# Performance work log

Hardware: AMD Instinct MI355X
Metric: run time of the kernel (lower is better)

## Reference

```python
import jax, jax.numpy as jnp
import numpy as np

VOCAB, EMB, NDIM, B, T = 50000, 300, 512, 128, 128


def gru_cell(x, h, Wih, Whh, bih, bhh):
    # torch nn.GRU gate order: [r, z, n]
    gi = x @ Wih.T + bih
    gh = h @ Whh.T + bhh
    i_r, i_z, i_n = jnp.split(gi, 3, axis=-1)
    h_r, h_z, h_n = jnp.split(gh, 3, axis=-1)
    r = jax.nn.sigmoid(i_r + h_r)
    z = jax.nn.sigmoid(i_z + h_z)
    n = jnp.tanh(i_n + r * h_n)
    return (1.0 - z) * n + z * h


def masked_gru(X, mask, h0, Wih, Whh, bih, bhh):
    # X: T x B x d, mask: T x B, h0: B x n. Replicates _gru_forward:
    # step-0 output is stored UNmasked (o_tm1 is None), later steps blend.
    h_raw = gru_cell(X[0], h0, Wih, Whh, bih, bhh)
    m0 = mask[0][:, None]
    h = h_raw * m0 + h0 * (1.0 - m0)
    o = h_raw

    def step(carry, inp):
        h, o = carry
        x_t, m_t = inp
        m = m_t[:, None]
        hr = gru_cell(x_t, h, Wih, Whh, bih, bhh)
        h_new = hr * m + h * (1.0 - m)
        o_new = hr * m + o * (1.0 - m)
        return (h_new, o_new), o_new

    (h_f, _), o_rest = jax.lax.scan(step, (h, o), (X[1:], mask[1:]))
    return jnp.concatenate([o[None], o_rest], axis=0), h_f


def rte_forward(premise, hypothesis, E, p_Wih, p_Whh, p_bih, p_bhh,
                h_Wih, h_Whh, h_bih, h_bhh, m_Wih, m_Whh, m_bih, m_bhh,
                W_y, W_h, W_r, W_alpha, out_W, out_b):
    bsz = premise.shape[0]
    n_dim = W_y.shape[0]
    mask_p = (premise != 0).astype(E.dtype).T            # T x B
    mask_h = (hypothesis != 0).astype(E.dtype).T
    enc_p = E[premise].transpose(1, 0, 2)                # T x B x EMB (eval: no dropout)
    enc_h = E[hypothesis].transpose(1, 0, 2)
    h0 = jnp.zeros((bsz, n_dim), dtype=E.dtype)
    o_p, h_n = masked_gru(enc_p, mask_p, h0, p_Wih, p_Whh, p_bih, p_bhh)
    o_h, _ = masked_gru(enc_h, mask_h, h_n, h_Wih, h_Whh, h_bih, h_bhh)

    Y = o_p.transpose(1, 0, 2)                           # B x Tp x n
    Yw = Y @ W_y                                         # hoisted: constant across steps
    maskY = mask_p.T                                     # B x Tp

    def step(r, inp):
        h_t, m_t = inp
        s = h_t @ W_h + r @ W_r                          # B x n
        M = jnp.tanh(Yw + s[:, None, :])                 # B x Tp x n
        alpha = (M @ W_alpha)[..., 0]                    # B x Tp
        alpha = alpha - 1000.0 * (1.0 - maskY)
        alpha = jax.nn.softmax(alpha, axis=-1)
        a = jnp.einsum('bt,btn->bn', alpha, Y)
        m_in = jnp.concatenate([a, h_t], axis=-1)        # B x 2n
        rr = gru_cell(m_in, r, m_Wih, m_Whh, m_bih, m_bhh)
        m = m_t[:, None]
        r_new = rr * m + r * (1.0 - m)
        return r_new, alpha

    r0 = jnp.zeros((bsz, n_dim), dtype=E.dtype)
    r_f, _alpha_vec = jax.lax.scan(step, r0, (o_h, mask_h))
    logits = r_f @ out_W.T + out_b                       # B x 3
    return jax.nn.log_softmax(logits, axis=-1)


def setup_inputs():
    key = jax.random.key(0)
    ks = jax.random.split(key, 22)
    s = 0.05
    def rn(k, sh):
        return jax.random.normal(k, sh, dtype=jnp.float32) * s
    G = 3 * NDIM
    return {
        "premise": jax.random.randint(ks[0], (B, T), 0, VOCAB),
        "hypothesis": jax.random.randint(ks[1], (B, T), 0, VOCAB),
        "E": rn(ks[2], (VOCAB, EMB)),
        "p_Wih": rn(ks[3], (G, EMB)), "p_Whh": rn(ks[4], (G, NDIM)),
        "p_bih": rn(ks[5], (G,)), "p_bhh": rn(ks[6], (G,)),
        "h_Wih": rn(ks[7], (G, EMB)), "h_Whh": rn(ks[8], (G, NDIM)),
        "h_bih": rn(ks[9], (G,)), "h_bhh": rn(ks[10], (G,)),
        "m_Wih": rn(ks[11], (G, 2 * NDIM)), "m_Whh": rn(ks[12], (G, NDIM)),
        "m_bih": rn(ks[13], (G,)), "m_bhh": rn(ks[14], (G,)),
        "W_y": rn(ks[15], (NDIM, NDIM)), "W_h": rn(ks[16], (NDIM, NDIM)),
        "W_r": rn(ks[17], (NDIM, NDIM)), "W_alpha": rn(ks[18], (NDIM, 1)),
        "out_W": rn(ks[19], (3, NDIM)), "out_b": rn(ks[20], (3,)),
    }


def reference(premise, hypothesis, E, p_Wih, p_Whh, p_bih, p_bhh,
              h_Wih, h_Whh, h_bih, h_bhh, m_Wih, m_Whh, m_bih, m_bhh,
              W_y, W_h, W_r, W_alpha, out_W, out_b):
    return rte_forward(premise, hypothesis, E, p_Wih, p_Whh, p_bih, p_bhh,
                       h_Wih, h_Whh, h_bih, h_bhh, m_Wih, m_Whh, m_bih, m_bhh,
                       W_y, W_h, W_r, W_alpha, out_W, out_b)
```

## Files before the change

### kernel.cpp

```cpp
#include <hip/hip_runtime.h>
#include <math.h>

#define B_SZ 128
#define T_SZ 128
#define EMBD 300
#define ND 512
#define G3 1536
#define FPAD 32

typedef short s16x8 __attribute__((ext_vector_type(8)));
typedef float f32x4 __attribute__((ext_vector_type(4)));
typedef unsigned long long u64;

__device__ __forceinline__ unsigned short f2b(float x) {
    unsigned u = __float_as_uint(x);
    unsigned r = (u + 0x7fff + ((u >> 16) & 1)) >> 16;
    return (unsigned short)r;
}
__device__ __forceinline__ float b2f(unsigned short v) {
    return __uint_as_float(((unsigned)v) << 16);
}
__device__ __forceinline__ float fsigmoid(float x) { return 1.0f / (1.0f + __expf(-x)); }
__device__ __forceinline__ float ftanh(float x) { return 1.0f - 2.0f / (__expf(2.0f * x) + 1.0f); }

__device__ __forceinline__ f32x4 mfma16(s16x8 a, s16x8 b, f32x4 c) {
    return __builtin_amdgcn_mfma_f32_16x16x32_bf16(a, b, c, 0, 0, 0);
}

__device__ __forceinline__ u64 cld64(const void* p) {
    return __hip_atomic_load((const u64*)p, __ATOMIC_RELAXED, __HIP_MEMORY_SCOPE_AGENT);
}
__device__ __forceinline__ void cst64(void* p, u64 v) {
    __hip_atomic_store((u64*)p, v, __ATOMIC_RELAXED, __HIP_MEMORY_SCOPE_AGENT);
}
__device__ __forceinline__ unsigned cld32(const void* p) {
    return __hip_atomic_load((const unsigned*)p, __ATOMIC_RELAXED, __HIP_MEMORY_SCOPE_AGENT);
}
__device__ __forceinline__ void cst32(void* p, unsigned v) {
    __hip_atomic_store((unsigned*)p, v, __ATOMIC_RELAXED, __HIP_MEMORY_SCOPE_AGENT);
}
__device__ __forceinline__ s16x8 cld_frag(const unsigned short* p) {
    union { u64 q[2]; s16x8 v; } u;
    u.q[0] = cld64(p);
    u.q[1] = cld64(p + 4);
    return u.v;
}

__device__ __forceinline__ void waitflags(const unsigned* f, int n, unsigned ep)
{
    if (threadIdx.x < 64) {
#pragma unroll 1
        for (int i = threadIdx.x; i < n; i += 64)
            while (cld32(&f[(long)i * FPAD]) < ep)
                __builtin_amdgcn_s_sleep(2);
    }
    __syncthreads();
}

__device__ __forceinline__ void fbar(unsigned* flags, int nb, unsigned ep)
{
    __syncthreads();
    if (threadIdx.x == 0)
        cst32(&flags[(long)blockIdx.x * FPAD], ep);
    waitflags(flags, nb, ep);
}

template<typename AT, bool OB>
__global__ __launch_bounds__(256)
void mfma_gemm(const AT* __restrict__ A, const int* __restrict__ idxA,
               const unsigned short* __restrict__ Wb, const float* __restrict__ bias,
               void* __restrict__ Cv,
               int M, int N, int K, int ldA, int Kpad, int ldC)
{
    __shared__ unsigned short As[64][40];
    __shared__ unsigned short Bs[64][40];
    const int tid = threadIdx.x;
    const int wv = tid >> 6, lane = tid & 63;
    const int wm = wv >> 1, wn = wv & 1;
    const int m0 = blockIdx.y * 64, n0 = blockIdx.x * 64;

    f32x4 acc[2][2] = {{{0.f,0.f,0.f,0.f},{0.f,0.f,0.f,0.f}},
                       {{0.f,0.f,0.f,0.f},{0.f,0.f,0.f,0.f}}};
    const int r_st = tid >> 2, k_st = (tid & 3) * 8;

    long arow = -1;
    {
        int gm = m0 + r_st;
        if (gm < M) arow = idxA ? (long)idxA[gm] : (long)gm;
    }

    const int kIters = (K + 31) / 32;
    for (int it = 0; it < kIters; ++it) {
        const int kg = it * 32 + k_st;
        {
            s16x8 pk = {0,0,0,0,0,0,0,0};
            if (arow >= 0) {
                if constexpr (sizeof(AT) == 2) {
                    if (kg + 8 <= K) {
                        pk = *(const s16x8*)((const unsigned short*)A + arow * (long)ldA + kg);
                    } else {
#pragma unroll
                        for (int j = 0; j < 8; ++j)
                            if (kg + j < K) pk[j] = (short)((const unsigned short*)A)[arow * (long)ldA + kg + j];
                    }
                } else {
                    if (kg + 8 <= K) {
                        const float* p = (const float*)A + arow * (long)ldA + kg;
                        f32x4 u0 = *(const f32x4*)p;
                        f32x4 u1 = *(const f32x4*)(p + 4);
#pragma unroll
                        for (int j = 0; j < 4; ++j) { pk[j] = (short)f2b(u0[j]); pk[4+j] = (short)f2b(u1[j]); }
                    } else {
#pragma unroll
                        for (int j = 0; j < 8; ++j) {
                            int kk = kg + j;
                            if (kk < K) pk[j] = (short)f2b(((const float*)A)[arow * (long)ldA + kk]);
                        }
                    }
                }
            }
            *(s16x8*)&As[r_st][k_st] = pk;
        }
        {
            int gn = n0 + r_st;
            s16x8 pk = {0,0,0,0,0,0,0,0};
            if (gn < N) pk = *(const s16x8*)&Wb[(long)gn * Kpad + kg];
            *(s16x8*)&Bs[r_st][k_st] = pk;
        }
        __syncthreads();
        {
            const int koff = (lane >> 4) * 8;
            s16x8 af[2], bfr[2];
#pragma unroll
            for (int f = 0; f < 2; ++f) {
                af[f]  = *(s16x8*)&As[wm * 32 + f * 16 + (lane & 15)][koff];
                bfr[f] = *(s16x8*)&Bs[wn * 32 + f * 16 + (lane & 15)][koff];
            }
#pragma unroll
            for (int fi = 0; fi < 2; ++fi)
#pragma unroll
                for (int fj = 0; fj < 2; ++fj)
                    acc[fi][fj] = mfma16(af[fi], bfr[fj], acc[fi][fj]);
        }
        __syncthreads();
    }
#pragma unroll
    for (int fi = 0; fi < 2; ++fi)
#pragma unroll
        for (int fj = 0; fj < 2; ++fj)
#pragma unroll
            for (int r = 0; r < 4; ++r) {
                int m = m0 + wm * 32 + fi * 16 + (lane >> 4) * 4 + r;
                int n = n0 + wn * 32 + fj * 16 + (lane & 15);
                if (m < M && n < N) {
                    float v = acc[fi][fj][r];
                    if (bias) v += bias[n];
                    if constexpr (OB) ((unsigned short*)Cv)[(long)m * ldC + n] = f2b(v);
                    else               ((float*)Cv)[(long)m * ldC + n] = v;
                }
            }
}

#define GRU_NB 64
__global__ __launch_bounds__(256, 1)
void gru_chain(const unsigned short* __restrict__ Whh_b, const float* __restrict__ GI,
               const float* __restrict__ bhh, const int* __restrict__ toks,
               float* __restrict__ h32a, float* __restrict__ h32b,
               unsigned short* __restrict__ h16a, unsigned short* __restrict__ h16b,
               unsigned short* __restrict__ o_bt,
               unsigned* __restrict__ flags)
{
    __shared__ unsigned short wlds[3][16][512];
    __shared__ unsigned short ht[64][20];
    const int tid = threadIdx.x;
    const int wv = tid >> 6, lane = tid & 63;
    const int dt = blockIdx.x & 31, bh = blockIdx.x >> 5;
    const int b0 = bh * 64;

    for (int s = 0; s < 12; ++s) {
        int slot = tid + s * 256;
        int g = slot >> 10, rem = slot & 1023, ks = rem >> 6, ln = rem & 63;
        int row = g * ND + dt * 16 + (ln & 15);
        int k = ks * 32 + (ln >> 4) * 8;
        *(s16x8*)&wlds[g][ks][ln * 8] = *(const s16x8*)&Whh_b[(long)row * ND + k];
    }
    __syncthreads();

    const int d = dt * 16 + (lane & 15);
    const int brow = b0 + wv * 16 + (lane >> 4) * 4;
    const int arow = b0 + wv * 16 + (lane & 15);
    const int akoff = (lane >> 4) * 8;

    float o_run[4] = {0.f, 0.f, 0.f, 0.f};
    unsigned ep = 0;

    for (int t = 0; t < T_SZ; ++t) {
        const unsigned short* hin16 = (t & 1) ? h16b : h16a;
        const float*          hin32 = (t & 1) ? h32b : h32a;
        float*          hout32 = (t & 1) ? h32a : h32b;
        unsigned short* hout16 = (t & 1) ? h16a : h16b;

        const float* git = GI + (long)t * (B_SZ * G3);
        float gi_r[4], gi_z[4], gi_n[4], hp[4]; int mk[4];
#pragma unroll
        for (int rr = 0; rr < 4; ++rr) {
            int b = brow + rr;
            gi_r[rr] = git[(long)b * G3 + d];
            gi_z[rr] = git[(long)b * G3 + ND + d];
            gi_n[rr] = git[(long)b * G3 + 2 * ND + d];
            hp[rr]   = hin32[(long)b * ND + d];
            mk[rr]   = toks[b * T_SZ + t];
        }

        f32x4 acc0 = {0,0,0,0}, acc1 = {0,0,0,0}, acc2 = {0,0,0,0};
#pragma unroll
        for (int ks = 0; ks < 16; ++ks) {
            s16x8 a  = cld_frag(&hin16[(long)arow * ND + ks * 32 + akoff]);
            s16x8 br = *(s16x8*)&wlds[0][ks][lane * 8];
            s16x8 bz = *(s16x8*)&wlds[1][ks][lane * 8];
            s16x8 bn = *(s16x8*)&wlds[2][ks][lane * 8];
            acc0 = mfma16(a, br, acc0);
            acc1 = mfma16(a, bz, acc1);
            acc2 = mfma16(a, bn, acc2);
        }

#pragma unroll
        for (int rr = 0; rr < 4; ++rr) {
            int b = brow + rr;
            float rg = fsigmoid(gi_r[rr] + acc0[rr] + bhh[d]);
            float zg = fsigmoid(gi_z[rr] + acc1[rr] + bhh[ND + d]);
            float ng = ftanh(gi_n[rr] + rg * (acc2[rr] + bhh[2 * ND + d]));
            float hr = (1.0f - zg) * ng + zg * hp[rr];
            bool m = mk[rr] != 0;
            float hn = m ? hr : hp[rr];
            hout32[(long)b * ND + d] = hn;
            ht[b - b0][lane & 15] = f2b(hn);
            o_run[rr] = (t == 0) ? hr : (m ? hr : o_run[rr]);
            o_bt[((long)b * T_SZ + t) * ND + d] = f2b(o_run[rr]);
        }
        __syncthreads();
        {
            int bl = tid & 63, dq = tid >> 6;
            u64 v = *(u64*)&ht[bl][dq * 4];
            cst64(&hout16[(long)(b0 + bl) * ND + dt * 16 + dq * 4], v);
        }
        fbar(flags, GRU_NB, ++ep);
    }
}

#define UP_NB 32
#define YPITCH 520
__global__ __launch_bounds__(256, 1)
void match_chain(const unsigned short* __restrict__ WrT_b,
                 const unsigned short* __restrict__ mWihL_b,
                 const unsigned short* __restrict__ mWhh_b,
                 const unsigned short* __restrict__ OHWh_bt,
                 const unsigned short* __restrict__ OHGI_bt,
                 const float* __restrict__ m_bhh, const float* __restrict__ Walpha,
                 const unsigned short* __restrict__ Yw_bb,
                 const unsigned short* __restrict__ Y_bb,
                 const int* __restrict__ prem, const int* __restrict__ hyp,
                 float* __restrict__ r32,
                 unsigned short* __restrict__ r16a, unsigned short* __restrict__ r16b,
                 unsigned short* __restrict__ a16, unsigned short* __restrict__ s16,
                 unsigned* __restrict__ lflags, unsigned* __restrict__ uflags,
                 unsigned* __restrict__ sflags)
{
    __shared__ __align__(16) unsigned char smem[157696];
    const int tid = threadIdx.x;
    const int wv = tid >> 6, lane = tid & 63;

    if (blockIdx.x < 128) {
        const int b = blockIdx.x;
        unsigned short (*ywl)[YPITCH] = (unsigned short(*)[YPITCH])smem;
        float* wal  = (float*)(smem + 133120);
        float* sarr = (float*)(smem + 135168);
        float* part = (float*)(smem + 137216);
        float* lg   = (float*)(smem + 138240);
        float* red  = (float*)(smem + 138752);
        float* sr2  = (float*)(smem + 138784);

        for (int s = 0; s < 32; ++s) {
            int c = s * 256 + tid;
            int row = c >> 6, cg = c & 63;
            *(s16x8*)&ywl[row][cg * 8] =
                *(const s16x8*)&Yw_bb[((long)b * T_SZ + row) * ND + cg * 8];
        }
        if (tid < 128) {
            f32x4 w = *(const f32x4*)&Walpha[tid * 4];
            *(f32x4*)&wal[tid * 4] = w;
        }
        __syncthreads();

        const int tp = tid >> 1, gh = tid & 1;
        const unsigned short* yrow = &ywl[tp][gh * 256];
        const float* sp  = &sarr[gh * 256];
        const float* wap = &wal[gh * 256];

        for (int t = 0; t < T_SZ; ++t) {
            waitflags(sflags, UP_NB, (unsigned)(t + 1));
            if (tid < 64) {
                s16x8 q = cld_frag(&s16[(long)b * ND + tid * 8]);
#pragma unroll
                for (int j = 0; j < 8; ++j) sarr[tid * 8 + j] = b2f((unsigned short)q[j]);
            }
            __syncthreads();
            {
                float acc = 0.f;
#pragma unroll 4
                for (int i8 = 0; i8 < 32; ++i8) {
                    s16x8 yw = *(const s16x8*)&yrow[i8 * 8];
                    f32x4 s0 = *(const f32x4*)&sp[i8 * 8];
                    f32x4 s1 = *(const f32x4*)&sp[i8 * 8 + 4];
                    f32x4 w0 = *(const f32x4*)&wap[i8 * 8];
                    f32x4 w1 = *(const f32x4*)&wap[i8 * 8 + 4];
#pragma unroll
                    for (int j = 0; j < 4; ++j)
                        acc += ftanh(b2f((unsigned short)yw[j]) + s0[j]) * w0[j];
#pragma unroll
                    for (int j = 0; j < 4; ++j)
                        acc += ftanh(b2f((unsigned short)yw[4 + j]) + s1[j]) * w1[j];
                }
                part[tid] = acc;
            }
            __syncthreads();
            if (tid < 128) {
                float v = part[tid * 2] + part[tid * 2 + 1];
                float mm = (prem[b * T_SZ + tid] != 0) ? 0.f : 1000.f;
                lg[tid] = v - mm;
            }
            __syncthreads();
            if (tid < 64) {
                float v = fmaxf(lg[tid], lg[tid + 64]);
#pragma unroll
                for (int off = 32; off; off >>= 1) v = fmaxf(v, __shfl_xor(v, off));
                if (tid == 0) red[0] = v;
            }
            __syncthreads();
            float mx = red[0];
            if (tid < T_SZ) lg[tid] = __expf(lg[tid] - mx);
            __syncthreads();
            if (tid < 64) {
                float v = lg[tid] + lg[tid + 64];
#pragma unroll
                for (int off = 32; off; off >>= 1) v += __shfl_xor(v, off);
                if (tid == 0) red[1] = v;
            }
            __syncthreads();
            float inv = 1.0f / red[1];
            int g = tid >> 7, lt = tid & 127, n4 = lt * 4;
            f32x4 acw = {0.f, 0.f, 0.f, 0.f};
#pragma unroll 8
            for (int i = 0; i < 64; ++i) {
                int tpp = g * 64 + i;
                float al = lg[tpp] * inv;
                u64 q = *(const u64*)&Y_bb[((long)b * T_SZ + tpp) * ND + n4];
                acw[0] += al * b2f((unsigned short)q);
                acw[1] += al * b2f((unsigned short)(q >> 16));
                acw[2] += al * b2f((unsigned short)(q >> 32));
                acw[3] += al * b2f((unsigned short)(q >> 48));
            }
            if (g == 1) *(f32x4*)&sr2[n4] = acw;
            __syncthreads();
            if (g == 0) {
                f32x4 o = *(f32x4*)&sr2[n4];
                u64 pk = (u64)f2b(acw[0] + o[0]) | ((u64)f2b(acw[1] + o[1]) << 16)
                       | ((u64)f2b(acw[2] + o[2]) << 32) | ((u64)f2b(acw[3] + o[3]) << 48);
                cst64(&a16[(long)b * ND + n4], pk);
            }
            __syncthreads();
            if (tid == 0) cst32(&lflags[(long)b * FPAD], (unsigned)(t + 1));
        }
    } else {
        const int ug = blockIdx.x - 128;
        unsigned short (*wA)[16][512] = (unsigned short(*)[16][512])smem;
        unsigned short (*wR)[16][512] = (unsigned short(*)[16][512])(smem + 49152);
        float (*bounce)[84] = (float(*)[84])(smem + 49152 + 65536);

        for (int s = 0; s < 12; ++s) {
            int slot = tid + s * 256;
            int fam = slot >> 10, rem = slot & 1023, ks = rem >> 6, ln = rem & 63;
            int row = fam * ND + ug * 16 + (ln & 15);
            int k = ks * 32 + (ln >> 4) * 8;
            *(s16x8*)&wA[fam][ks][ln * 8] = *(const s16x8*)&mWihL_b[(long)row * ND + k];
        }
        for (int s = 0; s < 16; ++s) {
            int slot = tid + s * 256;
            int fam = slot >> 10, rem = slot & 1023, ks = rem >> 6, ln = rem & 63;
            int k = ks * 32 + (ln >> 4) * 8;
            const unsigned short* src = (fam < 3)
                ? &mWhh_b[(long)(fam * ND + ug * 16 + (ln & 15)) * ND + k]
                : &WrT_b[(long)(ug * 16 + (ln & 15)) * ND + k];
            *(s16x8*)&wR[fam][ks][ln * 8] = *(const s16x8*)src;
        }
        __syncthreads();

        const int akoff = (lane >> 4) * 8;
        const int cb = tid >> 1;
        const int half = tid & 1;
        const int d0 = ug * 16 + half * 8;

        for (int t = 0; t < T_SZ; ++t) {
            waitflags(uflags, UP_NB, (unsigned)t);
            const unsigned short* r16rd = (t & 1) ? r16b : r16a;
            unsigned short*       r16wr = (t & 1) ? r16a : r16b;

            f32x4 aSR[2] = {{0,0,0,0},{0,0,0,0}}, aSZ[2] = {{0,0,0,0},{0,0,0,0}};
            f32x4 aHN[2] = {{0,0,0,0},{0,0,0,0}}, aS[2]  = {{0,0,0,0},{0,0,0,0}};
            f32x4 aGN[2] = {{0,0,0,0},{0,0,0,0}};
#pragma unroll
            for (int f = 0; f < 2; ++f) {
                int row = wv * 32 + f * 16 + (lane & 15);
#pragma unroll
                for (int ks = 0; ks < 16; ++ks) {
                    s16x8 a = cld_frag(&r16rd[(long)row * ND + ks * 32 + akoff]);
                    aSR[f] = mfma16(a, *(s16x8*)&wR[0][ks][lane * 8], aSR[f]);
                    aSZ[f] = mfma16(a, *(s16x8*)&wR[1][ks][lane * 8], aSZ[f]);
                    aHN[f] = mfma16(a, *(s16x8*)&wR[2][ks][lane * 8], aHN[f]);
                    aS[f]  = mfma16(a, *(s16x8*)&wR[3][ks][lane * 8], aS[f]);
                }
            }
#pragma unroll
            for (int f = 0; f < 2; ++f)
#pragma unroll
                for (int rr = 0; rr < 4; ++rr)
                    bounce[wv * 32 + f * 16 + (lane >> 4) * 4 + rr][64 + (lane & 15)] = aS[f][rr];
            __syncthreads();
            {
                u64 qa = *(const u64*)&OHWh_bt[((long)cb * T_SZ + t) * ND + d0];
                u64 qb = *(const u64*)&OHWh_bt[((long)cb * T_SZ + t) * ND + d0 + 4];
                u64 w0 = 0, w1 = 0;
#pragma unroll
                for (int j = 0; j < 4; ++j) {
                    float v0 = bounce[cb][64 + half * 8 + j]     + b2f((unsigned short)(qa >> (16 * j)));
                    float v1 = bounce[cb][64 + half * 8 + 4 + j] + b2f((unsigned short)(qb >> (16 * j)));
                    w0 |= (u64)f2b(v0) << (16 * j);
                    w1 |= (u64)f2b(v1) << (16 * j);
                }
                cst64(&s16[(long)cb * ND + d0], w0);
                cst64(&s16[(long)cb * ND + d0 + 4], w1);
            }
            __syncthreads();
            if (tid == 0) cst32(&sflags[(long)ug * FPAD], (unsigned)(t + 1));

            waitflags(lflags, 128, (unsigned)(t + 1));
#pragma unroll
            for (int f = 0; f < 2; ++f) {
                int row = wv * 32 + f * 16 + (lane & 15);
#pragma unroll
                for (int ks = 0; ks < 16; ++ks) {
                    s16x8 a = cld_frag(&a16[(long)row * ND + ks * 32 + akoff]);
                    aSR[f] = mfma16(a, *(s16x8*)&wA[0][ks][lane * 8], aSR[f]);
                    aSZ[f] = mfma16(a, *(s16x8*)&wA[1][ks][lane * 8], aSZ[f]);
                    aGN[f] = mfma16(a, *(s16x8*)&wA[2][ks][lane * 8], aGN[f]);
                }
            }
#pragma unroll
            for (int f = 0; f < 2; ++f)
#pragma unroll
                for (int rr = 0; rr < 4; ++rr) {
                    int bb = wv * 32 + f * 16 + (lane >> 4) * 4 + rr;
                    bounce[bb][0  + (lane & 15)] = aSR[f][rr];
                    bounce[bb][16 + (lane & 15)] = aSZ[f][rr];
                    bounce[bb][32 + (lane & 15)] = aGN[f][rr];
                    bounce[bb][48 + (lane & 15)] = aHN[f][rr];
                }
            __syncthreads();
            {
                const unsigned short* og = OHGI_bt + ((long)cb * T_SZ + t) * G3;
                u64 q0a = *(const u64*)&og[d0];            u64 q0b = *(const u64*)&og[d0 + 4];
                u64 q1a = *(const u64*)&og[ND + d0];       u64 q1b = *(const u64*)&og[ND + d0 + 4];
                u64 q2a = *(const u64*)&og[2 * ND + d0];   u64 q2b = *(const u64*)&og[2 * ND + d0 + 4];
                f32x4 rpA = *(const f32x4*)&r32[(long)cb * ND + d0];
                f32x4 rpB = *(const f32x4*)&r32[(long)cb * ND + d0 + 4];
                bool mkk = hyp[cb * T_SZ + t] != 0;
                u64 w0 = 0, w1 = 0;
#pragma unroll
                for (int j = 0; j < 8; ++j) {
                    int dl = half * 8 + j;
                    int dd = ug * 16 + dl;
                    u64 qg0 = (j < 4) ? q0a : q0b;
                    u64 qg1 = (j < 4) ? q1a : q1b;
                    u64 qg2 = (j < 4) ? q2a : q2b;
                    int sh = 16 * (j & 3);
                    float sr  = bounce[cb][0 + dl]  + b2f((unsigned short)(qg0 >> sh)) + m_bhh[dd];
                    float sz  = bounce[cb][16 + dl] + b2f((unsigned short)(qg1 >> sh)) + m_bhh[ND + dd];
                    float gin = bounce[cb][32 + dl] + b2f((unsigned short)(qg2 >> sh));
                    float ghn = bounce[cb][48 + dl] + m_bhh[2 * ND + dd];
                    float rg = fsigmoid(sr), zg = fsigmoid(sz);
                    float ng = ftanh(gin + rg * ghn);
                    float rp = (j < 4) ? rpA[j & 3] : rpB[j & 3];
                    float rn = (1.0f - zg) * ng + zg * rp;
                    float v = mkk ? rn : rp;
                    if (j < 4) rpA[j & 3] = v; else rpB[j & 3] = v;
                    if (j < 4) w0 |= (u64)f2b(v) << sh; else w1 |= (u64)f2b(v) << sh;
                }
                *(f32x4*)&r32[(long)cb * ND + d0] = rpA;
                *(f32x4*)&r32[(long)cb * ND + d0 + 4] = rpB;
                cst64(&r16wr[(long)cb * ND + d0], w0);
                cst64(&r16wr[(long)cb * ND + d0 + 4], w1);
            }
            __syncthreads();
            if (tid == 0) cst32(&uflags[(long)ug * FPAD], (unsigned)(t + 1));
        }
    }
}

__global__ void prep_idx(const int* __restrict__ prem, const int* __restrict__ hyp,
                         int* __restrict__ idx_p, int* __restrict__ idx_h)
{
    int i = blockIdx.x * blockDim.x + threadIdx.x;
    if (i < B_SZ * T_SZ) {
        int t = i / B_SZ, b = i % B_SZ;
        idx_p[i] = prem[b * T_SZ + t];
        idx_h[i] = hyp[b * T_SZ + t];
    }
}

__global__ void conv_w(const float* __restrict__ in, unsigned short* __restrict__ out,
                       int N, int K, int Kpad, int ldIn, int colOff)
{
    long i = (long)blockIdx.x * blockDim.x + threadIdx.x;
    if (i >= (long)N * Kpad) return;
    int n = (int)(i / Kpad), k = (int)(i % Kpad);
    float v = (k < K) ? in[(long)n * ldIn + k + colOff] : 0.0f;
    out[i] = f2b(v);
}

__global__ void conv_wT(const float* __restrict__ in, unsigned short* __restrict__ out,
                        int N, int K, int Kpad, int ldIn)
{
    long i = (long)blockIdx.x * blockDim.x + threadIdx.x;
    if (i >= (long)N * Kpad) return;
    int n = (int)(i / Kpad), k = (int)(i % Kpad);
    float v = (k < K) ? in[(long)k * ldIn + n] : 0.0f;
    out[i] = f2b(v);
}

__global__ void zero_kernel(float* __restrict__ p, int n)
{
    int i = blockIdx.x * blockDim.x + threadIdx.x;
    if (i < n) p[i] = 0.0f;
}

__global__ void final_logits(const float* __restrict__ r, const float* __restrict__ outW,
                             const float* __restrict__ outb, float* __restrict__ out)
{
    int b = blockIdx.x;
    int lane = threadIdx.x;
    float a0 = 0.0f, a1 = 0.0f, a2 = 0.0f;
    for (int k = lane; k < ND; k += 64) {
        float rv = r[(long)b * ND + k];
        a0 += rv * outW[0 * ND + k];
        a1 += rv * outW[1 * ND + k];
        a2 += rv * outW[2 * ND + k];
    }
#pragma unroll
    for (int off = 32; off; off >>= 1) {
        a0 += __shfl_down(a0, off);
        a1 += __shfl_down(a1, off);
        a2 += __shfl_down(a2, off);
    }
    if (lane == 0) {
        float l0 = a0 + outb[0], l1 = a1 + outb[1], l2 = a2 + outb[2];
        float mx = fmaxf(l0, fmaxf(l1, l2));
        float se = expf(l0 - mx) + expf(l1 - mx) + expf(l2 - mx);
        float ls = mx + logf(se);
        out[b * 3 + 0] = l0 - ls;
        out[b * 3 + 1] = l1 - ls;
        out[b * 3 + 2] = l2 - ls;
    }
}

extern "C" void kernel_launch(void* const* d_in, const int* in_sizes, int n_in,
                              void* d_out, int out_size, void* d_ws, size_t ws_size,
                              hipStream_t stream)
{
    const int*   prem    = (const int*)d_in[0];
    const int*   hyp     = (const int*)d_in[1];
    const float* E       = (const float*)d_in[2];
    const float* p_Wih   = (const float*)d_in[3];
    const float* p_Whh   = (const float*)d_in[4];
    const float* p_bih   = (const float*)d_in[5];
    const float* p_bhh   = (const float*)d_in[6];
    const float* h_Wih   = (const float*)d_in[7];
    const float* h_Whh   = (const float*)d_in[8];
    const float* h_bih   = (const float*)d_in[9];
    const float* h_bhh   = (const float*)d_in[10];
    const float* m_Wih   = (const float*)d_in[11];
    const float* m_Whh   = (const float*)d_in[12];
    const float* m_bih   = (const float*)d_in[13];
    const float* m_bhh   = (const float*)d_in[14];
    const float* W_y     = (const float*)d_in[15];
    const float* W_h     = (const float*)d_in[16];
    const float* W_r     = (const float*)d_in[17];
    const float* W_alpha = (const float*)d_in[18];
    const float* out_W   = (const float*)d_in[19];
    const float* out_b   = (const float*)d_in[20];
    float* out = (float*)d_out;

    const int MB = T_SZ * B_SZ;
    const int NFLAGS = 320 * FPAD;

    float* ws = (float*)d_ws;
    size_t off = 0;
    float* GI    = ws + off; off += (size_t)MB * G3;
    float* h32a  = ws + off; off += (size_t)B_SZ * ND;
    float* h32b  = ws + off; off += (size_t)B_SZ * ND;
    float* r32   = ws + off; off += (size_t)B_SZ * ND;
    unsigned* flags = (unsigned*)(ws + off); off += NFLAGS;
    int* idx_p = (int*)(ws + off); off += (size_t)B_SZ * T_SZ;
    int* idx_h = (int*)(ws + off); off += (size_t)B_SZ * T_SZ;
    unsigned short* ub = (unsigned short*)(ws + off);
    size_t uoff = 0;
    unsigned short* o_p_bt = ub + uoff; uoff += (size_t)MB * ND;
    unsigned short* o_h_bt = ub + uoff; uoff += (size_t)MB * ND;
    unsigned short* Yw_bb  = ub + uoff; uoff += (size_t)MB * ND;
    unsigned short* OHWh_bt= ub + uoff; uoff += (size_t)MB * ND;
    unsigned short* OHGI_bt= ub + uoff; uoff += (size_t)MB * G3;
    unsigned short* h16a   = ub + uoff; uoff += (size_t)B_SZ * ND;
    unsigned short* h16b   = ub + uoff; uoff += (size_t)B_SZ * ND;
    unsigned short* r16a   = ub + uoff; uoff += (size_t)B_SZ * ND;
    unsigned short* r16b   = ub + uoff; uoff += (size_t)B_SZ * ND;
    unsigned short* a16    = ub + uoff; uoff += (size_t)B_SZ * ND;
    unsigned short* s16    = ub + uoff; uoff += (size_t)B_SZ * ND;
    unsigned short* pWih_b = ub + uoff; uoff += (size_t)G3 * 320;
    unsigned short* hWih_b = ub + uoff; uoff += (size_t)G3 * 320;
    unsigned short* pWhh_b = ub + uoff; uoff += (size_t)G3 * ND;
    unsigned short* hWhh_b = ub + uoff; uoff += (size_t)G3 * ND;
    unsigned short* mWihL_b= ub + uoff; uoff += (size_t)G3 * ND;
    unsigned short* mWihR  = ub + uoff; uoff += (size_t)G3 * ND;
    unsigned short* mWhh_b = ub + uoff; uoff += (size_t)G3 * ND;
    unsigned short* WyT_b  = ub + uoff; uoff += (size_t)ND * ND;
    unsigned short* WhT_b  = ub + uoff; uoff += (size_t)ND * ND;
    unsigned short* WrT_b  = ub + uoff; uoff += (size_t)ND * ND;
    off += (uoff + 1) / 2;
    if (ws_size < off * sizeof(float)) return;

    auto cblk = [](long n) { return (int)((n + 255) / 256); };

    prep_idx<<<cblk(MB), 256, 0, stream>>>(prem, hyp, idx_p, idx_h);
    conv_w <<<cblk((long)G3 * 320), 256, 0, stream>>>(p_Wih, pWih_b, G3, EMBD, 320, EMBD, 0);
    conv_w <<<cblk((long)G3 * 320), 256, 0, stream>>>(h_Wih, hWih_b, G3, EMBD, 320, EMBD, 0);
    conv_w <<<cblk((long)G3 * ND), 256, 0, stream>>>(p_Whh, pWhh_b, G3, ND, ND, ND, 0);
    conv_w <<<cblk((long)G3 * ND), 256, 0, stream>>>(h_Whh, hWhh_b, G3, ND, ND, ND, 0);
    conv_w <<<cblk((long)G3 * ND), 256, 0, stream>>>(m_Wih, mWihL_b, G3, ND, ND, 2 * ND, 0);
    conv_w <<<cblk((long)G3 * ND), 256, 0, stream>>>(m_Wih, mWihR, G3, ND, ND, 2 * ND, ND);
    conv_w <<<cblk((long)G3 * ND), 256, 0, stream>>>(m_Whh, mWhh_b, G3, ND, ND, ND, 0);
    conv_wT<<<cblk((long)ND * ND), 256, 0, stream>>>(W_y, WyT_b, ND, ND, ND, ND);
    conv_wT<<<cblk((long)ND * ND), 256, 0, stream>>>(W_h, WhT_b, ND, ND, ND, ND);
    conv_wT<<<cblk((long)ND * ND), 256, 0, stream>>>(W_r, WrT_b, ND, ND, ND, ND);
    zero_kernel<<<cblk(B_SZ * ND), 256, 0, stream>>>(h32a, B_SZ * ND);
    zero_kernel<<<cblk(B_SZ * ND / 2), 256, 0, stream>>>((float*)h16a, B_SZ * ND / 2);
    zero_kernel<<<cblk(B_SZ * ND), 256, 0, stream>>>(r32, B_SZ * ND);
    zero_kernel<<<cblk(B_SZ * ND / 2), 256, 0, stream>>>((float*)r16a, B_SZ * ND / 2);
    zero_kernel<<<cblk(B_SZ * ND / 2), 256, 0, stream>>>((float*)r16b, B_SZ * ND / 2);
    zero_kernel<<<cblk(NFLAGS), 256, 0, stream>>>((float*)flags, NFLAGS);

    {
        dim3 g(G3 / 64, MB / 64);
        mfma_gemm<float, false><<<g, 256, 0, stream>>>(E, idx_p, pWih_b, p_bih, GI,
                                                       MB, G3, EMBD, EMBD, 320, G3);
    }
    gru_chain<<<GRU_NB, 256, 0, stream>>>(pWhh_b, GI, p_bhh, prem, h32a, h32b, h16a, h16b,
                                          o_p_bt, &flags[0]);

    {
        dim3 g(G3 / 64, MB / 64);
        mfma_gemm<float, false><<<g, 256, 0, stream>>>(E, idx_h, hWih_b, h_bih, GI,
                                                       MB, G3, EMBD, EMBD, 320, G3);
    }
    gru_chain<<<GRU_NB, 256, 0, stream>>>(hWhh_b, GI, h_bhh, hyp, h32a, h32b, h16a, h16b,
                                          o_h_bt, &flags[64 * FPAD]);

    {
        dim3 g(ND / 64, MB / 64);
        mfma_gemm<unsigned short, true><<<g, 256, 0, stream>>>(o_p_bt, nullptr, WyT_b, nullptr,
                                                               Yw_bb, MB, ND, ND, ND, ND, ND);
        mfma_gemm<unsigned short, true><<<g, 256, 0, stream>>>(o_h_bt, nullptr, WhT_b, nullptr,
                                                               OHWh_bt, MB, ND, ND, ND, ND, ND);
        dim3 g2(G3 / 64, MB / 64);
        mfma_gemm<unsigned short, true><<<g2, 256, 0, stream>>>(o_h_bt, nullptr, mWihR, m_bih,
                                                                OHGI_bt, MB, G3, ND, ND, ND, G3);
    }

    match_chain<<<160, 256, 0, stream>>>(WrT_b, mWihL_b, mWhh_b, OHWh_bt, OHGI_bt,
                                         m_bhh, W_alpha, Yw_bb, o_p_bt, prem, hyp,
                                         r32, r16a, r16b, a16, s16,
                                         &flags[128 * FPAD], &flags[256 * FPAD],
                                         &flags[288 * FPAD]);

    final_logits<<<B_SZ, 64, 0, stream>>>(r32, out_W, out_b, out);
}
```

Before: 7.348 ms.

## Replicate barrier flags, keep recurrent state in registers, prefetch step inputs

Each block now posts its barrier flag to eight replicated flag arrays and polls only its own replica. This spreads the spin-wait traffic on shared cache lines that sits on the critical path of every recurrent step. The GRU and match-update hidden states stay in registers and are written to global memory only at the final step. The match kernel drops the max-subtraction from its softmax, folds normalisation into the weighted sum, and hoists the mask. OHWh/OHGI are stored time-major so their loads can be issued before the wait; dropping the max-subtraction risks exp overflow for large logits.

```diff
diff --git a/kernel.cpp b/kernel.cpp
--- a/kernel.cpp
+++ b/kernel.cpp
@@ -7,6 +7,8 @@
 #define ND 512
 #define G3 1536
 #define FPAD 32
+#define NFID 320
+#define NREP 8
 
 typedef short s16x8 __attribute__((ext_vector_type(8)));
 typedef float f32x4 __attribute__((ext_vector_type(4)));
@@ -46,31 +48,42 @@
     return u.v;
 }
 
-__device__ __forceinline__ void waitflags(const unsigned* f, int n, unsigned ep)
-{
+__device__ __forceinline__ void postflag(unsigned* flags, int base, int id, unsigned ep)
+{
+    if (threadIdx.x < NREP)
+        cst32(&flags[((long)threadIdx.x * NFID + base + id) * FPAD], ep);
+}
+__device__ __forceinline__ void waitflags(const unsigned* flags, int base, int n,
+                                          unsigned ep, int rep)
+{
+    const unsigned* fr = flags + (long)rep * NFID * FPAD;
     if (threadIdx.x < 64) {
 #pragma unroll 1
         for (int i = threadIdx.x; i < n; i += 64)
-            while (cld32(&f[(long)i * FPAD]) < ep)
+            while (cld32(&fr[(long)(base + i) * FPAD]) < ep)
                 __builtin_amdgcn_s_sleep(2);
     }
     __syncthreads();
 }
-
-__device__ __forceinline__ void fbar(unsigned* flags, int nb, unsigned ep)
+__device__ __forceinline__ void fbar(unsigned* flags, int base, int nb, unsigned ep)
 {
     __syncthreads();
-    if (threadIdx.x == 0)
-        cst32(&flags[(long)blockIdx.x * FPAD], ep);
-    waitflags(flags, nb, ep);
-}
+    postflag(flags, base, blockIdx.x & 63, ep);
+    waitflags(flags, base, nb, ep, blockIdx.x & 7);
+}
+
+#define FB_GRUP 0
+#define FB_GRUH 64
+#define FB_LF   128
+#define FB_UF   256
+#define FB_SF   288
 
 template<typename AT, bool OB>
 __global__ __launch_bounds__(256)
 void mfma_gemm(const AT* __restrict__ A, const int* __restrict__ idxA,
                const unsigned short* __restrict__ Wb, const float* __restrict__ bias,
                void* __restrict__ Cv,
-               int M, int N, int K, int ldA, int Kpad, int ldC)
+               int M, int N, int K, int ldA, int Kpad, int ldC, int permC)
 {
     __shared__ unsigned short As[64][40];
     __shared__ unsigned short Bs[64][40];
@@ -155,8 +168,9 @@
                 if (m < M && n < N) {
                     float v = acc[fi][fj][r];
                     if (bias) v += bias[n];
-                    if constexpr (OB) ((unsigned short*)Cv)[(long)m * ldC + n] = f2b(v);
-                    else               ((float*)Cv)[(long)m * ldC + n] = v;
+                    long mo = permC ? ((long)(m & 127) * B_SZ + (m >> 7)) : (long)m;
+                    if constexpr (OB) ((unsigned short*)Cv)[mo * ldC + n] = f2b(v);
+                    else               ((float*)Cv)[mo * ldC + n] = v;
                 }
             }
 }
@@ -165,10 +179,10 @@
 __global__ __launch_bounds__(256, 1)
 void gru_chain(const unsigned short* __restrict__ Whh_b, const float* __restrict__ GI,
                const float* __restrict__ bhh, const int* __restrict__ toks,
-               float* __restrict__ h32a, float* __restrict__ h32b,
+               float* __restrict__ h32,
                unsigned short* __restrict__ h16a, unsigned short* __restrict__ h16b,
                unsigned short* __restrict__ o_bt,
-               unsigned* __restrict__ flags)
+               unsigned* __restrict__ flags, int fbase)
 {
     __shared__ unsigned short wlds[3][16][512];
     __shared__ unsigned short ht[64][20];
@@ -191,24 +205,25 @@
     const int arow = b0 + wv * 16 + (lane & 15);
     const int akoff = (lane >> 4) * 8;
 
+    float hreg[4];
+#pragma unroll
+    for (int rr = 0; rr < 4; ++rr) hreg[rr] = h32[(long)(brow + rr) * ND + d];
+
     float o_run[4] = {0.f, 0.f, 0.f, 0.f};
     unsigned ep = 0;
 
     for (int t = 0; t < T_SZ; ++t) {
         const unsigned short* hin16 = (t & 1) ? h16b : h16a;
-        const float*          hin32 = (t & 1) ? h32b : h32a;
-        float*          hout32 = (t & 1) ? h32a : h32b;
         unsigned short* hout16 = (t & 1) ? h16a : h16b;
 
         const float* git = GI + (long)t * (B_SZ * G3);
-        float gi_r[4], gi_z[4], gi_n[4], hp[4]; int mk[4];
+        float gi_r[4], gi_z[4], gi_n[4]; int mk[4];
 #pragma unroll
         for (int rr = 0; rr < 4; ++rr) {
             int b = brow + rr;
             gi_r[rr] = git[(long)b * G3 + d];
             gi_z[rr] = git[(long)b * G3 + ND + d];
             gi_n[rr] = git[(long)b * G3 + 2 * ND + d];
-            hp[rr]   = hin32[(long)b * ND + d];
             mk[rr]   = toks[b * T_SZ + t];
         }
 
@@ -230,11 +245,12 @@
             float rg = fsigmoid(gi_r[rr] + acc0[rr] + bhh[d]);
             float zg = fsigmoid(gi_z[rr] + acc1[rr] + bhh[ND + d]);
             float ng = ftanh(gi_n[rr] + rg * (acc2[rr] + bhh[2 * ND + d]));
-            float hr = (1.0f - zg) * ng + zg * hp[rr];
+            float hr = (1.0f - zg) * ng + zg * hreg[rr];
             bool m = mk[rr] != 0;
-            float hn = m ? hr : hp[rr];
-            hout32[(long)b * ND + d] = hn;
+            float hn = m ? hr : hreg[rr];
+            hreg[rr] = hn;
             ht[b - b0][lane & 15] = f2b(hn);
+            if (t == T_SZ - 1) h32[(long)b * ND + d] = hn;
             o_run[rr] = (t == 0) ? hr : (m ? hr : o_run[rr]);
             o_bt[((long)b * T_SZ + t) * ND + d] = f2b(o_run[rr]);
         }
@@ -244,18 +260,18 @@
             u64 v = *(u64*)&ht[bl][dq * 4];
             cst64(&hout16[(long)(b0 + bl) * ND + dt * 16 + dq * 4], v);
         }
-        fbar(flags, GRU_NB, ++ep);
+        fbar(flags, fbase, GRU_NB, ++ep);
     }
 }
 
 #define UP_NB 32
-#define YPITCH 520
+#define YPITCH 536
 __global__ __launch_bounds__(256, 1)
 void match_chain(const unsigned short* __restrict__ WrT_b,
                  const unsigned short* __restrict__ mWihL_b,
                  const unsigned short* __restrict__ mWhh_b,
-                 const unsigned short* __restrict__ OHWh_bt,
-                 const unsigned short* __restrict__ OHGI_bt,
+                 const unsigned short* __restrict__ OHWh_tb,
+                 const unsigned short* __restrict__ OHGI_tb,
                  const float* __restrict__ m_bhh, const float* __restrict__ Walpha,
                  const unsigned short* __restrict__ Yw_bb,
                  const unsigned short* __restrict__ Y_bb,
@@ -263,8 +279,7 @@
                  float* __restrict__ r32,
                  unsigned short* __restrict__ r16a, unsigned short* __restrict__ r16b,
                  unsigned short* __restrict__ a16, unsigned short* __restrict__ s16,
-                 unsigned* __restrict__ lflags, unsigned* __restrict__ uflags,
-                 unsigned* __restrict__ sflags)
+                 unsigned* __restrict__ flags)
 {
     __shared__ __align__(16) unsigned char smem[157696];
     const int tid = threadIdx.x;
@@ -272,13 +287,14 @@
 
     if (blockIdx.x < 128) {
         const int b = blockIdx.x;
+        const int rep = b & 7;
         unsigned short (*ywl)[YPITCH] = (unsigned short(*)[YPITCH])smem;
-        float* wal  = (float*)(smem + 133120);
-        float* sarr = (float*)(smem + 135168);
-        float* part = (float*)(smem + 137216);
-        float* lg   = (float*)(smem + 138240);
-        float* red  = (float*)(smem + 138752);
-        float* sr2  = (float*)(smem + 138784);
+        float* wal  = (float*)(smem + 137216);
+        float* sarr = (float*)(smem + 139264);
+        float* part = (float*)(smem + 141312);
+        float* lg   = (float*)(smem + 142336);
+        float* red  = (float*)(smem + 142848);
+        float* sr2  = (float*)(smem + 142880);
 
         for (int s = 0; s < 32; ++s) {
             int c = s * 256 + tid;
@@ -290,15 +306,18 @@
             f32x4 w = *(const f32x4*)&Walpha[tid * 4];
             *(f32x4*)&wal[tid * 4] = w;
         }
+        float mmreg = 0.f;
+        if (tid < 128) mmreg = (prem[b * T_SZ + tid] != 0) ? 0.f : 1000.f;
         __syncthreads();
 
         const int tp = tid >> 1, gh = tid & 1;
         const unsigned short* yrow = &ywl[tp][gh * 256];
         const float* sp  = &sarr[gh * 256];
         const float* wap = &wal[gh * 256];
+        const int g = tid >> 7, lt = tid & 127, n4 = lt * 4;
 
         for (int t = 0; t < T_SZ; ++t) {
-            waitflags(sflags, UP_NB, (unsigned)(t + 1));
+            waitflags(flags, FB_SF, UP_NB, (unsigned)(t + 1), rep);
             if (tid < 64) {
                 s16x8 q = cld_frag(&s16[(long)b * ND + tid * 8]);
 #pragma unroll
@@ -324,55 +343,39 @@
                 part[tid] = acc;
             }
             __syncthreads();
-            if (tid < 128) {
-                float v = part[tid * 2] + part[tid * 2 + 1];
-                float mm = (prem[b * T_SZ + tid] != 0) ? 0.f : 1000.f;
-                lg[tid] = v - mm;
-            }
-            __syncthreads();
-            if (tid < 64) {
-                float v = fmaxf(lg[tid], lg[tid + 64]);
-#pragma unroll
-                for (int off = 32; off; off >>= 1) v = fmaxf(v, __shfl_xor(v, off));
-                if (tid == 0) red[0] = v;
-            }
-            __syncthreads();
-            float mx = red[0];
-            if (tid < T_SZ) lg[tid] = __expf(lg[tid] - mx);
-            __syncthreads();
-            if (tid < 64) {
-                float v = lg[tid] + lg[tid + 64];
-#pragma unroll
-                for (int off = 32; off; off >>= 1) v += __shfl_xor(v, off);
-                if (tid == 0) red[1] = v;
-            }
-            __syncthreads();
-            float inv = 1.0f / red[1];
-            int g = tid >> 7, lt = tid & 127, n4 = lt * 4;
+            if (tid < 128) lg[tid] = __expf(part[tid * 2] + part[tid * 2 + 1] - mmreg);
+            __syncthreads();
+            float suml = 0.f;
             f32x4 acw = {0.f, 0.f, 0.f, 0.f};
 #pragma unroll 8
             for (int i = 0; i < 64; ++i) {
                 int tpp = g * 64 + i;
-                float al = lg[tpp] * inv;
+                float al = lg[tpp];
+                suml += al;
                 u64 q = *(const u64*)&Y_bb[((long)b * T_SZ + tpp) * ND + n4];
                 acw[0] += al * b2f((unsigned short)q);
                 acw[1] += al * b2f((unsigned short)(q >> 16));
                 acw[2] += al * b2f((unsigned short)(q >> 32));
                 acw[3] += al * b2f((unsigned short)(q >> 48));
             }
-            if (g == 1) *(f32x4*)&sr2[n4] = acw;
+            if (g == 1) {
+                *(f32x4*)&sr2[n4] = acw;
+                if (lt == 0) red[0] = suml;
+            }
             __syncthreads();
             if (g == 0) {
+                float inv = 1.0f / (suml + red[0]);
                 f32x4 o = *(f32x4*)&sr2[n4];
-                u64 pk = (u64)f2b(acw[0] + o[0]) | ((u64)f2b(acw[1] + o[1]) << 16)
-                       | ((u64)f2b(acw[2] + o[2]) << 32) | ((u64)f2b(acw[3] + o[3]) << 48);
+                u64 pk = (u64)f2b((acw[0] + o[0]) * inv) | ((u64)f2b((acw[1] + o[1]) * inv) << 16)
+                       | ((u64)f2b((acw[2] + o[2]) * inv) << 32) | ((u64)f2b((acw[3] + o[3]) * inv) << 48);
                 cst64(&a16[(long)b * ND + n4], pk);
             }
             __syncthreads();
-            if (tid == 0) cst32(&lflags[(long)b * FPAD], (unsigned)(t + 1));
+            postflag(flags, FB_LF, b, (unsigned)(t + 1));
         }
     } else {
         const int ug = blockIdx.x - 128;
+        const int rep = ug & 7;
         unsigned short (*wA)[16][512] = (unsigned short(*)[16][512])smem;
         unsigned short (*wR)[16][512] = (unsigned short(*)[16][512])(smem + 49152);
         float (*bounce)[84] = (float(*)[84])(smem + 49152 + 65536);
@@ -400,8 +403,19 @@
         const int half = tid & 1;
         const int d0 = ug * 16 + half * 8;
 
+        f32x4 rpA = {0,0,0,0}, rpB = {0,0,0,0};
+
         for (int t = 0; t < T_SZ; ++t) {
-            waitflags(uflags, UP_NB, (unsigned)t);
+            const unsigned short* ohw = &OHWh_tb[((long)t * B_SZ + cb) * ND + d0];
+            u64 qa = *(const u64*)ohw;
+            u64 qb = *(const u64*)(ohw + 4);
+            const unsigned short* og = &OHGI_tb[((long)t * B_SZ + cb) * G3];
+            u64 q0a = *(const u64*)&og[d0];            u64 q0b = *(const u64*)&og[d0 + 4];
+            u64 q1a = *(const u64*)&og[ND + d0];       u64 q1b = *(const u64*)&og[ND + d0 + 4];
+            u64 q2a = *(const u64*)&og[2 * ND + d0];   u64 q2b = *(const u64*)&og[2 * ND + d0 + 4];
+            int hv = hyp[cb * T_SZ + t];
+
+            waitflags(flags, FB_UF, UP_NB, (unsigned)t, rep);
             const unsigned short* r16rd = (t & 1) ? r16b : r16a;
             unsigned short*       r16wr = (t & 1) ? r16a : r16b;
 
@@ -427,8 +441,6 @@
                     bounce[wv * 32 + f * 16 + (lane >> 4) * 4 + rr][64 + (lane & 15)] = aS[f][rr];
             __syncthreads();
             {
-                u64 qa = *(const u64*)&OHWh_bt[((long)cb * T_SZ + t) * ND + d0];
-                u64 qb = *(const u64*)&OHWh_bt[((long)cb * T_SZ + t) * ND + d0 + 4];
                 u64 w0 = 0, w1 = 0;
 #pragma unroll
                 for (int j = 0; j < 4; ++j) {
@@ -441,9 +453,9 @@
                 cst64(&s16[(long)cb * ND + d0 + 4], w1);
             }
             __syncthreads();
-            if (tid == 0) cst32(&sflags[(long)ug * FPAD], (unsigned)(t + 1));
-
-            waitflags(lflags, 128, (unsigned)(t + 1));
+            postflag(flags, FB_SF, ug, (unsigned)(t + 1));
+
+            waitflags(flags, FB_LF, 128, (unsigned)(t + 1), rep);
 #pragma unroll
             for (int f = 0; f < 2; ++f) {
                 int row = wv * 32 + f * 16 + (lane & 15);
@@ -467,13 +479,7 @@
                 }
             __syncthreads();
             {
-                const unsigned short* og = OHGI_bt + ((long)cb * T_SZ + t) * G3;
-                u64 q0a = *(const u64*)&og[d0];            u64 q0b = *(const u64*)&og[d0 + 4];
-                u64 q1a = *(const u64*)&og[ND + d0];       u64 q1b = *(const u64*)&og[ND + d0 + 4];
-                u64 q2a = *(const u64*)&og[2 * ND + d0];   u64 q2b = *(const u64*)&og[2 * ND + d0 + 4];
-                f32x4 rpA = *(const f32x4*)&r32[(long)cb * ND + d0];
-                f32x4 rpB = *(const f32x4*)&r32[(long)cb * ND + d0 + 4];
-                bool mkk = hyp[cb * T_SZ + t] != 0;
+                bool mkk = hv != 0;
                 u64 w0 = 0, w1 = 0;
 #pragma unroll
                 for (int j = 0; j < 8; ++j) {
@@ -495,13 +501,15 @@
                     if (j < 4) rpA[j & 3] = v; else rpB[j & 3] = v;
                     if (j < 4) w0 |= (u64)f2b(v) << sh; else w1 |= (u64)f2b(v) << sh;
                 }
-                *(f32x4*)&r32[(long)cb * ND + d0] = rpA;
-                *(f32x4*)&r32[(long)cb * ND + d0 + 4] = rpB;
+                if (t == T_SZ - 1) {
+                    *(f32x4*)&r32[(long)cb * ND + d0] = rpA;
+                    *(f32x4*)&r32[(long)cb * ND + d0 + 4] = rpB;
+                }
                 cst64(&r16wr[(long)cb * ND + d0], w0);
                 cst64(&r16wr[(long)cb * ND + d0 + 4], w1);
             }
             __syncthreads();
-            if (tid == 0) cst32(&uflags[(long)ug * FPAD], (unsigned)(t + 1));
+            postflag(flags, FB_UF, ug, (unsigned)(t + 1));
         }
     }
 }
@@ -600,13 +608,12 @@
     float* out = (float*)d_out;
 
     const int MB = T_SZ * B_SZ;
-    const int NFLAGS = 320 * FPAD;
+    const int NFLAGS = NREP * NFID * FPAD;
 
     float* ws = (float*)d_ws;
     size_t off = 0;
     float* GI    = ws + off; off += (size_t)MB * G3;
-    float* h32a  = ws + off; off += (size_t)B_SZ * ND;
-    float* h32b  = ws + off; off += (size_t)B_SZ * ND;
+    float* h32   = ws + off; off += (size_t)B_SZ * ND;
     float* r32   = ws + off; off += (size_t)B_SZ * ND;
     unsigned* flags = (unsigned*)(ws + off); off += NFLAGS;
     int* idx_p = (int*)(ws + off); off += (size_t)B_SZ * T_SZ;
@@ -616,8 +623,8 @@
     unsigned short* o_p_bt = ub + uoff; uoff += (size_t)MB * ND;
     unsigned short* o_h_bt = ub + uoff; uoff += (size_t)MB * ND;
     unsigned short* Yw_bb  = ub + uoff; uoff += (size_t)MB * ND;
-    unsigned short* OHWh_bt= ub + uoff; uoff += (size_t)MB * ND;
-    unsigned short* OHGI_bt= ub + uoff; uoff += (size_t)MB * G3;
+    unsigned short* OHWh_tb= ub + uoff; uoff += (size_t)MB * ND;
+    unsigned short* OHGI_tb= ub + uoff; uoff += (size_t)MB * G3;
     unsigned short* h16a   = ub + uoff; uoff += (size_t)B_SZ * ND;
     unsigned short* h16b   = ub + uoff; uoff += (size_t)B_SZ * ND;
     unsigned short* r16a   = ub + uoff; uoff += (size_t)B_SZ * ND;
@@ -650,7 +657,7 @@
     conv_wT<<<cblk((long)ND * ND), 256, 0, stream>>>(W_y, WyT_b, ND, ND, ND, ND);
     conv_wT<<<cblk((long)ND * ND), 256, 0, stream>>>(W_h, WhT_b, ND, ND, ND, ND);
     conv_wT<<<cblk((long)ND * ND), 256, 0, stream>>>(W_r, WrT_b, ND, ND, ND, ND);
-    zero_kernel<<<cblk(B_SZ * ND), 256, 0, stream>>>(h32a, B_SZ * ND);
+    zero_kernel<<<cblk(B_SZ * ND), 256, 0, stream>>>(h32, B_SZ * ND);
     zero_kernel<<<cblk(B_SZ * ND / 2), 256, 0, stream>>>((float*)h16a, B_SZ * ND / 2);
     zero_kernel<<<cblk(B_SZ * ND), 256, 0, stream>>>(r32, B_SZ * ND);
     zero_kernel<<<cblk(B_SZ * ND / 2), 256, 0, stream>>>((float*)r16a, B_SZ * ND / 2);
@@ -660,35 +667,33 @@
     {
         dim3 g(G3 / 64, MB / 64);
         mfma_gemm<float, false><<<g, 256, 0, stream>>>(E, idx_p, pWih_b, p_bih, GI,
-                                                       MB, G3, EMBD, EMBD, 320, G3);
-    }
-    gru_chain<<<GRU_NB, 256, 0, stream>>>(pWhh_b, GI, p_bhh, prem, h32a, h32b, h16a, h16b,
-                                          o_p_bt, &flags[0]);
+                                                       MB, G3, EMBD, EMBD, 320, G3, 0);
+    }
+    gru_chain<<<GRU_NB, 256, 0, stream>>>(pWhh_b, GI, p_bhh, prem, h32, h16a, h16b,
+                                          o_p_bt, flags, FB_GRUP);
 
     {
         dim3 g(G3 / 64, MB / 64);
         mfma_gemm<float, false><<<g, 256, 0, stream>>>(E, idx_h, hWih_b, h_bih, GI,
-                                                       MB, G3, EMBD, EMBD, 320, G3);
-    }
-    gru_chain<<<GRU_NB, 256, 0, stream>>>(hWhh_b, GI, h_bhh, hyp, h32a, h32b, h16a, h16b,
-                                          o_h_bt, &flags[64 * FPAD]);
+                                                       MB, G3, EMBD, EMBD, 320, G3, 0);
+    }
+    gru_chain<<<GRU_NB, 256, 0, stream>>>(hWhh_b, GI, h_bhh, hyp, h32, h16a, h16b,
+                                          o_h_bt, flags, FB_GRUH);
 
     {
         dim3 g(ND / 64, MB / 64);
         mfma_gemm<unsigned short, true><<<g, 256, 0, stream>>>(o_p_bt, nullptr, WyT_b, nullptr,
-                                                               Yw_bb, MB, ND, ND, ND, ND, ND);
+                                                               Yw_bb, MB, ND, ND, ND, ND, ND, 0);
         mfma_gemm<unsigned short, true><<<g, 256, 0, stream>>>(o_h_bt, nullptr, WhT_b, nullptr,
-                                                               OHWh_bt, MB, ND, ND, ND, ND, ND);
+                                                               OHWh_tb, MB, ND, ND, ND, ND, ND, 1);
         dim3 g2(G3 / 64, MB / 64);
         mfma_gemm<unsigned short, true><<<g2, 256, 0, stream>>>(o_h_bt, nullptr, mWihR, m_bih,
-                                                                OHGI_bt, MB, G3, ND, ND, ND, G3);
-    }
-
-    match_chain<<<160, 256, 0, stream>>>(WrT_b, mWihL_b, mWhh_b, OHWh_bt, OHGI_bt,
+                                                                OHGI_tb, MB, G3, ND, ND, ND, G3, 1);
+    }
+
+    match_chain<<<160, 256, 0, stream>>>(WrT_b, mWihL_b, mWhh_b, OHWh_tb, OHGI_tb,
                                          m_bhh, W_alpha, Yw_bb, o_p_bt, prem, hyp,
-                                         r32, r16a, r16b, a16, s16,
-                                         &flags[128 * FPAD], &flags[256 * FPAD],
-                                         &flags[288 * FPAD]);
+                                         r32, r16a, r16b, a16, s16, flags);
 
     final_logits<<<B_SZ, 64, 0, stream>>>(r32, out_W, out_b, out);
 }
```

Measured after the change: 7.025 ms. -4.4%, faster.
